# Performance work log

Hardware: AMD Instinct MI355X
Metric: run time of the kernel (lower is better)

The kernel has to match this reference:

```python
import jax, jax.numpy as jnp
import numpy as np

D = 512          # descriptor_dim
H = 8            # num_heads
HD = D // H      # per-head dim
L = 12           # GNN layers: ['self','cross']*6
NAMES = ['self', 'cross'] * 6
SINKHORN_ITERS = 100
IN_EPS = 1e-5    # InstanceNorm1d eps


def _conv1x1(W, b, x):
    # W: [o, d], b: [o], x: [b, d, n] -> [b, o, n]  (1x1 Conv1d)
    return jnp.einsum('od,bdn->bon', W, x) + b[:, None]


def _instance_norm(x):
    # InstanceNorm1d(affine=False): normalize each (batch, channel) over n
    mean = jnp.mean(x, axis=-1, keepdims=True)
    var = jnp.mean(jnp.square(x - mean), axis=-1, keepdims=True)  # biased
    return (x - mean) * jax.lax.rsqrt(var + IN_EPS)


def _mha(x, src, Wq, bq, Wk, bk, Wv, bv, Wm, bm):
    # x, src: [b, D, n] / [b, D, m]; fused head-major QKV projections
    b, _, n = x.shape
    m = src.shape[2]
    q = _conv1x1(Wq, bq, x).reshape(b, H, HD, n)
    k = _conv1x1(Wk, bk, src).reshape(b, H, HD, m)
    v = _conv1x1(Wv, bv, src).reshape(b, H, HD, m)
    scores = jnp.einsum('bhdn,bhdm->bhnm', q, k) / np.float32(np.sqrt(HD))
    prob = jax.nn.softmax(scores, axis=-1)
    out = jnp.einsum('bhnm,bhdm->bhdn', prob, v)      # [b, h, hd, n]
    # torch stacks heads at dim=2 -> [b, hd, h, n], then views (b, hd*h, n):
    out = out.transpose(0, 2, 1, 3).reshape(b, D, n)  # dim-major merge order
    return _conv1x1(Wm, bm, out)


def _prop_layer(x, src, Wq, bq, Wk, bk, Wv, bv, Wm, bm, W1, b1, W2, b2):
    # AttentionalPropagation: attn message + MLP([2D, 2D, D]) with InstanceNorm
    msg = _mha(x, src, Wq, bq, Wk, bk, Wv, bv, Wm, bm)
    y = jnp.concatenate([x, msg], axis=1)             # [b, 2D, n]
    z = jax.nn.relu(_instance_norm(_conv1x1(W1, b1, y)))
    return _conv1x1(W2, b2, z)                        # [b, D, n]


def _log_optimal_transport(scores, alpha, iters):
    b, m, n = scores.shape
    ms = jnp.asarray(m, scores.dtype)
    ns = jnp.asarray(n, scores.dtype)
    bins0 = jnp.broadcast_to(alpha, (b, m, 1))
    bins1 = jnp.broadcast_to(alpha, (b, 1, n))
    a = jnp.broadcast_to(alpha, (b, 1, 1))
    couplings = jnp.concatenate(
        [jnp.concatenate([scores, bins0], -1),
         jnp.concatenate([bins1, a], -1)], 1)         # [b, m+1, n+1]
    norm = -jnp.log(ms + ns)
    log_mu = jnp.concatenate([jnp.full((m,), norm), (jnp.log(ns) + norm)[None]])
    log_nu = jnp.concatenate([jnp.full((n,), norm), (jnp.log(ms) + norm)[None]])
    log_mu = jnp.broadcast_to(log_mu, (b, m + 1))
    log_nu = jnp.broadcast_to(log_nu, (b, n + 1))

    def step(carry, _):
        u, v = carry
        u = log_mu - jax.scipy.special.logsumexp(couplings + v[:, None, :], axis=2)
        v = log_nu - jax.scipy.special.logsumexp(couplings + u[:, :, None], axis=1)
        return (u, v), None

    (u, v), _ = jax.lax.scan(
        step, (jnp.zeros_like(log_mu), jnp.zeros_like(log_nu)), None,
        length=iters)
    return couplings + u[:, :, None] + v[:, None, :] - norm


def setup_inputs() -> dict:
    key = jax.random.key(0)
    ks = jax.random.split(key, 12)
    B, N0, N1 = 4, 1024, 1024
    s = np.float32(0.03)  # ~1/sqrt(D) init scale for stability over 12 layers

    def p(k, shape):
        return jax.random.normal(k, shape, jnp.float32) * s

    return {
        'descs_0': jax.random.normal(ks[0], (B, N0, D), jnp.float32),
        'descs_1': jax.random.normal(ks[1], (B, N1, D), jnp.float32),
        'Wq': p(ks[2], (L, D, D)), 'bq': jnp.zeros((L, D), jnp.float32),
        'Wk': p(ks[3], (L, D, D)), 'bk': jnp.zeros((L, D), jnp.float32),
        'Wv': p(ks[4], (L, D, D)), 'bv': jnp.zeros((L, D), jnp.float32),
        'Wm': p(ks[5], (L, D, D)), 'bm': jnp.zeros((L, D), jnp.float32),
        'W1': p(ks[6], (L, 2 * D, 2 * D)), 'b1': jnp.zeros((L, 2 * D), jnp.float32),
        'W2': p(ks[7], (L, D, 2 * D)), 'b2': jnp.zeros((L, D), jnp.float32),
        'Wf': p(ks[8], (D, D)), 'bf': jnp.zeros((D,), jnp.float32),
        'bin_score': jnp.asarray(1.0, jnp.float32),
    }


def reference(descs_0, descs_1, Wq, bq, Wk, bk, Wv, bv, Wm, bm,
              W1, b1, W2, b2, Wf, bf, bin_score):
    # [B, N, D] -> channels-first [B, D, N]
    x0 = jnp.transpose(descs_0, (0, 2, 1))
    x1 = jnp.transpose(descs_1, (0, 2, 1))
    for i, name in enumerate(NAMES):
        s0, s1 = (x1, x0) if name == 'cross' else (x0, x1)
        args = (Wq[i], bq[i], Wk[i], bk[i], Wv[i], bv[i], Wm[i], bm[i],
                W1[i], b1[i], W2[i], b2[i])
        d0 = _prop_layer(x0, s0, *args)
        d1 = _prop_layer(x1, s1, *args)
        x0 = x0 + d0
        x1 = x1 + d1
    m0 = _conv1x1(Wf, bf, x0)
    m1 = _conv1x1(Wf, bf, x1)
    scores = jnp.einsum('bdn,bdm->bnm', m0, m1) / np.float32(np.sqrt(D))
    return _log_optimal_transport(scores, bin_score, SINKHORN_ITERS)
```

## Files before the change

kernel.cpp:

```cpp
#include <hip/hip_runtime.h>
#include <hip/hip_bf16.h>
#include <hip/hip_fp16.h>
#include <cmath>

using bf16 = __hip_bfloat16;
typedef __attribute__((ext_vector_type(8))) short short8;
typedef __attribute__((ext_vector_type(4))) float floatx4;
typedef unsigned long long u64t;

__device__ __forceinline__ void lds_load16(void* lds, const void* g) {
  __builtin_amdgcn_global_load_lds(
      (const __attribute__((address_space(1))) void*)g,
      (__attribute__((address_space(3))) void*)lds, 16, 0, 0);
}

struct GemmP {
  const bf16* A; const bf16* B;
  int M, N, K, lda, ldb;
  long sAimg, sAh, sBimg, sBh;
  int ZH, cross;
  float scale;
  const float* bias;
  float* Cf; int ldcf; long sCfImg, sCfH;
  bf16* Cb; int ldcb; long sCbImg, sCbH;
  __half* Ch; int ldch; long sChImg, sChH;
  const float* resid;
};

template <int NTILE>
__global__ __launch_bounds__(256, 2)
void gemm_bt(GemmP p) {
  __shared__ __align__(16) bf16 As[128 * 32];
  __shared__ __align__(16) bf16 Bs[NTILE * 32];
  constexpr int MI = (NTILE == 128) ? 4 : 2;
  const int z = blockIdx.z;
  const int imgA = z / p.ZH;
  const int h = z - imgA * p.ZH;
  const int imgB = imgA ^ p.cross;
  const bf16* Ab = p.A + (long)imgA * p.sAimg + (long)h * p.sAh;
  const bf16* Bb = p.B + (long)imgB * p.sBimg + (long)h * p.sBh;
  const int m0 = blockIdx.y * 128, n0 = blockIdx.x * NTILE;
  const int t = threadIdx.x, w = t >> 6, l = t & 63;
  const int lr = l >> 2, lk = (l & 3) * 8;
  const int fr = l & 15, fk = (l >> 4) * 8;

  const bf16* aG0 = Ab + (long)(m0 + w * 16 + lr) * p.lda + lk;
  const bf16* aG1 = aG0 + (long)64 * p.lda;
  const bf16* bG0 = Bb + (long)(n0 + w * 16 + lr) * p.ldb + lk;
  const bf16* bG1 = bG0 + (long)64 * p.ldb;
  bf16* aL0 = &As[w * 16 * 32];
  bf16* aL1 = &As[(w + 4) * 16 * 32];
  bf16* bL0 = &Bs[w * 16 * 32];
  bf16* bL1 = &Bs[(w + 4) * 16 * 32];
  const int wr = (NTILE == 128) ? (w >> 1) * 64 : w * 32;
  const int wc = (NTILE == 128) ? (w & 1) * 64 : 0;

  floatx4 zero4 = {0.f, 0.f, 0.f, 0.f};
  floatx4 acc[MI][4];
#pragma unroll
  for (int i = 0; i < MI; i++)
#pragma unroll
    for (int j = 0; j < 4; j++) acc[i][j] = zero4;

  for (int k0 = 0; k0 < p.K; k0 += 32) {
    lds_load16(aL0, aG0 + k0);
    lds_load16(aL1, aG1 + k0);
    lds_load16(bL0, bG0 + k0);
    if (NTILE == 128) lds_load16(bL1, bG1 + k0);
    __syncthreads();
    short8 af[MI], bfv[4];
#pragma unroll
    for (int i = 0; i < MI; i++)
      af[i] = *(const short8*)&As[(wr + i * 16 + fr) * 32 + fk];
#pragma unroll
    for (int j = 0; j < 4; j++)
      bfv[j] = *(const short8*)&Bs[(wc + j * 16 + fr) * 32 + fk];
#pragma unroll
    for (int i = 0; i < MI; i++)
#pragma unroll
      for (int j = 0; j < 4; j++)
        acc[i][j] = __builtin_amdgcn_mfma_f32_16x16x32_bf16(af[i], bfv[j], acc[i][j], 0, 0, 0);
    __syncthreads();
  }

  const int cl = l & 15, rq = (l >> 4) * 4;
  const long cfBase = (long)imgA * p.sCfImg + (long)h * p.sCfH;
  const long cbBase = (long)imgA * p.sCbImg + (long)h * p.sCbH;
  const long chBase = (long)imgA * p.sChImg + (long)h * p.sChH;
#pragma unroll
  for (int j = 0; j < 4; j++) {
    const int col = n0 + wc + j * 16 + cl;
    if (col >= p.N) continue;
    const float bv = p.bias ? p.bias[col] : 0.f;
#pragma unroll
    for (int i = 0; i < MI; i++) {
#pragma unroll
      for (int r = 0; r < 4; r++) {
        const int row = m0 + wr + i * 16 + rq + r;
        float val = acc[i][j][r] * p.scale + bv;
        if (p.resid) val += p.resid[cfBase + (long)row * p.ldcf + col];
        if (p.Cf) p.Cf[cfBase + (long)row * p.ldcf + col] = val;
        if (p.Cb) p.Cb[cbBase + (long)row * p.ldcb + col] = __float2bfloat16(val);
        if (p.Ch) p.Ch[chBase + (long)row * p.ldch + col] = __float2half(val);
      }
    }
  }
}

__global__ __launch_bounds__(256, 2)
void attn_fused(const bf16* __restrict__ QKV, const bf16* __restrict__ vchan,
                bf16* __restrict__ Yb, int cross) {
  __shared__ __align__(16) bf16 Qs[128 * 64];
  __shared__ __align__(16) bf16 Ks[64 * 64];
  __shared__ __align__(16) bf16 Vs[64 * 64];
  __shared__ __align__(16) bf16 Ps[128 * 64];
  const int z = blockIdx.z;
  const int img = z >> 3, h = z & 7;
  const int imgB = img ^ cross;
  const int q0 = blockIdx.x * 128;
  const int t = threadIdx.x, w = t >> 6, l = t & 63;
  const int g = l >> 4, fr = l & 15;
  const int wr = w * 32;

  {
    const bf16* src = QKV + ((long)(img * 1024 + q0)) * 1536 + h * 64;
#pragma unroll
    for (int k = 0; k < 4; k++) {
      const int chunk = t + k * 256;
      const int row = chunk >> 3, c16 = chunk & 7;
      const short8 vd = *(const short8*)(src + (long)row * 1536 + c16 * 8);
      *(short8*)((char*)Qs + row * 128 + ((c16 * 16) ^ ((row & 7) << 4))) = vd;
    }
  }
  __syncthreads();

  short8 qf[2][2];
#pragma unroll
  for (int i = 0; i < 2; i++)
#pragma unroll
    for (int ks = 0; ks < 2; ks++) {
      const int row = wr + i * 16 + fr;
      qf[i][ks] = *(const short8*)((const char*)Qs + row * 128 +
                                   ((ks * 64 + g * 16) ^ ((row & 7) << 4)));
    }

  floatx4 zero4 = {0.f, 0.f, 0.f, 0.f};
  floatx4 Oa[2][4];
  float m_run[2][4], l_run[2][4];
#pragma unroll
  for (int i = 0; i < 2; i++)
#pragma unroll
    for (int r = 0; r < 4; r++) { m_run[i][r] = -3.0e38f; l_run[i][r] = 0.f; }
#pragma unroll
  for (int i = 0; i < 2; i++)
#pragma unroll
    for (int jd = 0; jd < 4; jd++) Oa[i][jd] = zero4;

  const bf16* ksrc0 = QKV + ((long)(imgB * 1024)) * 1536 + 512 + h * 64;
  const bf16* vsrc0 = vchan + (long)imgB * 524288 + (long)(h * 64) * 1024;

  for (int kv = 0; kv < 16; kv++) {
    const int kv0 = kv * 64;
#pragma unroll
    for (int k = 0; k < 2; k++) {
      const int ch = t + k * 256;
      const int row = ch >> 3, c16 = ch & 7;
      const short8 vd = *(const short8*)(ksrc0 + (long)(kv0 + row) * 1536 + c16 * 8);
      *(short8*)((char*)Ks + row * 128 + ((c16 * 16) ^ ((row & 7) << 4))) = vd;
    }
#pragma unroll
    for (int k = 0; k < 2; k++) {
      const int ch = t + k * 256;
      const int row = ch >> 3, c16 = ch & 7;
      const short8 vd = *(const short8*)(vsrc0 + (long)row * 1024 + kv0 + c16 * 8);
      *(short8*)((char*)Vs + row * 128 + ((c16 * 16) ^ ((row & 7) << 4))) = vd;
    }
    __syncthreads();

    floatx4 sa[2][4];
#pragma unroll
    for (int i = 0; i < 2; i++)
#pragma unroll
      for (int j = 0; j < 4; j++) sa[i][j] = zero4;
    short8 bk[4][2];
#pragma unroll
    for (int j = 0; j < 4; j++)
#pragma unroll
      for (int ks = 0; ks < 2; ks++) {
        const int row = j * 16 + fr;
        bk[j][ks] = *(const short8*)((const char*)Ks + row * 128 +
                                     ((ks * 64 + g * 16) ^ ((row & 7) << 4)));
      }
#pragma unroll
    for (int i = 0; i < 2; i++)
#pragma unroll
      for (int j = 0; j < 4; j++)
#pragma unroll
        for (int ks = 0; ks < 2; ks++)
          sa[i][j] = __builtin_amdgcn_mfma_f32_16x16x32_bf16(qf[i][ks], bk[j][ks], sa[i][j], 0, 0, 0);

#pragma unroll
    for (int i = 0; i < 2; i++) {
#pragma unroll
      for (int r = 0; r < 4; r++) {
        float mx = -3.0e38f;
#pragma unroll
        for (int j = 0; j < 4; j++) {
          sa[i][j][r] *= 0.125f;
          mx = fmaxf(mx, sa[i][j][r]);
        }
#pragma unroll
        for (int o = 1; o < 16; o <<= 1) mx = fmaxf(mx, __shfl_xor(mx, o));
        const float mnew = fmaxf(m_run[i][r], mx);
        const float corr = __expf(m_run[i][r] - mnew);
        m_run[i][r] = mnew;
        float ps = 0.f;
#pragma unroll
        for (int j = 0; j < 4; j++) {
          const float pv = __expf(sa[i][j][r] - mnew);
          sa[i][j][r] = pv;
          ps += pv;
        }
#pragma unroll
        for (int o = 1; o < 16; o <<= 1) ps += __shfl_xor(ps, o);
        l_run[i][r] = l_run[i][r] * corr + ps;
#pragma unroll
        for (int jd = 0; jd < 4; jd++) Oa[i][jd][r] *= corr;
      }
    }

#pragma unroll
    for (int i = 0; i < 2; i++)
#pragma unroll
      for (int j = 0; j < 4; j++)
#pragma unroll
        for (int r = 0; r < 4; r++) {
          const int row = wr + i * 16 + g * 4 + r;
          const int colB = j * 32 + fr * 2;
          *(bf16*)((char*)Ps + row * 128 + (colB ^ ((row & 7) << 4))) =
              __float2bfloat16(sa[i][j][r]);
        }

    short8 pf[2][2], vf[4][2];
#pragma unroll
    for (int i = 0; i < 2; i++)
#pragma unroll
      for (int ks = 0; ks < 2; ks++) {
        const int row = wr + i * 16 + fr;
        pf[i][ks] = *(const short8*)((const char*)Ps + row * 128 +
                                     ((ks * 64 + g * 16) ^ ((row & 7) << 4)));
      }
#pragma unroll
    for (int jd = 0; jd < 4; jd++)
#pragma unroll
      for (int ks = 0; ks < 2; ks++) {
        const int row = jd * 16 + fr;
        vf[jd][ks] = *(const short8*)((const char*)Vs + row * 128 +
                                      ((ks * 64 + g * 16) ^ ((row & 7) << 4)));
      }
#pragma unroll
    for (int i = 0; i < 2; i++)
#pragma unroll
      for (int jd = 0; jd < 4; jd++)
#pragma unroll
        for (int ks = 0; ks < 2; ks++)
          Oa[i][jd] = __builtin_amdgcn_mfma_f32_16x16x32_bf16(pf[i][ks], vf[jd][ks], Oa[i][jd], 0, 0, 0);
    __syncthreads();
  }

#pragma unroll
  for (int i = 0; i < 2; i++) {
#pragma unroll
    for (int r = 0; r < 4; r++) {
      const float inv = 1.f / l_run[i][r];
      const int qrow = q0 + wr + i * 16 + g * 4 + r;
      bf16* dst = Yb + ((long)img * 1024 + qrow) * 1024 + 512 + h * 64;
#pragma unroll
      for (int jd = 0; jd < 4; jd++)
        dst[jd * 16 + fr] = __float2bfloat16(Oa[i][jd][r] * inv);
    }
  }
}

__global__ __launch_bounds__(256)
void cvt_f2b(const float* __restrict__ in, bf16* __restrict__ out, long n) {
  long i = (long)blockIdx.x * 256 + threadIdx.x;
  const long stride = (long)gridDim.x * 256;
  for (; i < n; i += stride) out[i] = __float2bfloat16(in[i]);
}

__global__ __launch_bounds__(256)
void cvt_prep(const float* __restrict__ W1, const float* __restrict__ Wm,
              bf16* __restrict__ w1r, bf16* __restrict__ wmT) {
  const long i = (long)blockIdx.x * 256 + threadIdx.x;
  if (i < 6291456L) {
    const int lay = (int)(i >> 19);
    const long r = i & 524287;
    const int o = (int)(r >> 9), k = (int)(r & 511);
    w1r[i] = __float2bfloat16(W1[(long)lay * 1048576 + (long)o * 1024 + 512 + k]);
  } else if (i < 9437184L) {
    const long j = i - 6291456L;
    const int lay = (int)(j >> 18);
    const long r = j & 262143;
    const int c = (int)(r >> 9), ii = (int)(r & 511);
    wmT[j] = __float2bfloat16(Wm[(long)lay * 262144 + (long)ii * 512 + (c & 63) * 8 + (c >> 6)]);
  }
}

__global__ __launch_bounds__(256)
void bc_calc(const float* __restrict__ W1, const float* __restrict__ bm,
             const float* __restrict__ b1, float* __restrict__ bc) {
  const int w = threadIdx.x >> 6, l = threadIdx.x & 63;
  const int og = blockIdx.x * 4 + w;
  const int lay = og >> 10, o = og & 1023;
  const float* wrow = W1 + (long)lay * 1048576 + (long)o * 1024 + 512;
  const float* bmr = bm + lay * 512;
  float s = 0.f;
#pragma unroll
  for (int j = 0; j < 8; j++) s += wrow[l + 64 * j] * bmr[l + 64 * j];
#pragma unroll
  for (int o2 = 32; o2 >= 1; o2 >>= 1) s += __shfl_xor(s, o2);
  if (l == 0) bc[og] = b1[og] + s;
}

__global__ __launch_bounds__(256)
void cvt_layer(const float* __restrict__ Wq, const float* __restrict__ Wk,
               const float* __restrict__ Wv, const float* __restrict__ W1,
               const float* __restrict__ W2, const bf16* __restrict__ wcAll,
               const float* __restrict__ bq, const float* __restrict__ bk,
               const float* __restrict__ bv,
               int layer, bf16* __restrict__ out, float* __restrict__ bqkv) {
  const long i = (long)blockIdx.x * 256 + threadIdx.x;
  if (i >= 2359296L + 1536) return;
  if (i >= 2359296L) {
    const int j = (int)(i - 2359296L);
    float b;
    if (j < 512) b = bq[layer * 512 + j];
    else if (j < 1024) b = bk[layer * 512 + j - 512];
    else b = bv[layer * 512 + j - 1024];
    bqkv[j] = b;
    return;
  }
  if (i < 786432) {
    float v;
    if (i < 262144) v = Wq[(long)layer * 262144 + i];
    else if (i < 524288) v = Wk[(long)layer * 262144 + i - 262144];
    else v = Wv[(long)layer * 262144 + i - 524288];
    out[i] = __float2bfloat16(v);
  } else if (i < 1835008) {
    const long j = i - 786432;
    const int o = (int)(j >> 10), k = (int)(j & 1023);
    if (k < 512)
      out[i] = __float2bfloat16(W1[(long)layer * 1048576 + (long)o * 1024 + k]);
    else
      out[i] = wcAll[(long)layer * 524288 + (long)o * 512 + (k - 512)];
  } else {
    const long j = i - 1835008;
    out[i] = __float2bfloat16(W2[(long)layer * 524288 + j]);
  }
}

__global__ __launch_bounds__(256)
void init_x(const float* __restrict__ d0, const float* __restrict__ d1,
            float* __restrict__ Xf, bf16* __restrict__ Yb) {
  long i = (long)blockIdx.x * 256 + threadIdx.x;
  const long stride = (long)gridDim.x * 256;
  const long n = 8L * 1024 * 512;
  for (; i < n; i += stride) {
    const int d = (int)(i & 511);
    const long nn = i >> 9;
    const int img = (int)(nn >> 10);
    const int row = (int)(nn & 1023);
    const int b = img >> 1, s = img & 1;
    const float v = (s ? d1 : d0)[((long)b * 1024 + row) * 512 + d];
    Xf[i] = v;
    Yb[(nn << 10) + d] = __float2bfloat16(v);
  }
}

__global__ __launch_bounds__(256)
void transpose_2b(const unsigned short* __restrict__ in, int ldi,
                  unsigned short* __restrict__ out) {
  __shared__ unsigned short tile[64][65];
  const int img = blockIdx.z;
  const int m0 = blockIdx.y * 64, c0 = blockIdx.x * 64;
  const int col = threadIdx.x & 63, r0 = threadIdx.x >> 6;
  const unsigned short* ip = in + ((long)img * 1024 + m0) * ldi + c0;
#pragma unroll
  for (int i = 0; i < 16; i++) { int r = r0 + i * 4; tile[r][col] = ip[(long)r * ldi + col]; }
  __syncthreads();
  unsigned short* op = out + ((long)img * 512 + c0) * 1024 + m0;
#pragma unroll
  for (int i = 0; i < 16; i++) { int r = r0 + i * 4; op[(long)r * 1024 + col] = tile[col][r]; }
}

__global__ __launch_bounds__(256)
void in_stats(const float* __restrict__ T1, float* __restrict__ stats) {
  const int img = blockIdx.z;
  const int c = blockIdx.x * 256 + threadIdx.x;
  const int nb = blockIdx.y;
  const float* p = T1 + ((long)img * 1024 + nb * 128) * 1024 + c;
  float s = 0.f, s2 = 0.f;
#pragma unroll 4
  for (int i = 0; i < 128; i++) { const float x = p[(long)i * 1024]; s += x; s2 += x * x; }
  atomicAdd(&stats[img * 2048 + c], s);
  atomicAdd(&stats[img * 2048 + 1024 + c], s2);
}

__global__ __launch_bounds__(256)
void in_apply(const float* __restrict__ T1, const float* __restrict__ stats,
              bf16* __restrict__ Z) {
  long i = (long)blockIdx.x * 256 + threadIdx.x;
  const long stride = (long)gridDim.x * 256;
  for (; i < 8L * 1024 * 1024; i += stride) {
    const int c = (int)(i & 1023);
    const int img = (int)(i >> 20);
    const float mean = stats[img * 2048 + c] * (1.f / 1024.f);
    const float var = fmaxf(stats[img * 2048 + 1024 + c] * (1.f / 1024.f) - mean * mean, 0.f);
    const float zz = (T1[i] - mean) * rsqrtf(var + 1e-5f);
    Z[i] = __float2bfloat16(fmaxf(zz, 0.f));
  }
}

__global__ __launch_bounds__(256)
void coup_to_fp16(float* __restrict__ io, const float* __restrict__ alpha,
                  __half* __restrict__ outN, __half* __restrict__ outT) {
  __shared__ float tile[32][33];
  const float a = *alpha;
  const int b = blockIdx.z;
  const int x0 = blockIdx.x * 32, y0 = blockIdx.y * 32;
  const int lx = threadIdx.x & 31, ly = threadIdx.x >> 5;
#pragma unroll
  for (int i = 0; i < 4; i++) {
    const int y = ly + i * 8;
    if (y0 + y < 1025 && x0 + lx < 1025) {
      const long idx = ((long)b * 1025 + y0 + y) * 1025 + x0 + lx;
      const bool edge = (y0 + y == 1024) || (x0 + lx == 1024);
      float vv;
      if (edge) { vv = a; io[idx] = a; }
      else vv = io[idx];
      tile[y][lx] = vv;
      outN[idx] = __float2half(vv);
    }
  }
  __syncthreads();
#pragma unroll
  for (int i = 0; i < 4; i++) {
    const int y = ly + i * 8;
    if (x0 + y < 1025 && y0 + lx < 1025)
      outT[((long)b * 1025 + x0 + y) * 1025 + y0 + lx] = __float2half(tile[lx][y]);
  }
}

#define SK_BLOCKS 256

#define SK_ROUND(CREG, CLAST, XREG, XLAST, SRC, DST)                            \
  {                                                                             \
    u64t pr;                                                                    \
    while ((unsigned)((pr = __hip_atomic_load(&(SRC)[t], __ATOMIC_RELAXED,      \
                                              __HIP_MEMORY_SCOPE_AGENT)) >>    \
                      32) != tag)                                               \
      __builtin_amdgcn_s_sleep(1);                                              \
    sv[t] = __uint_as_float((unsigned)pr);                                      \
    if (t == 0) {                                                               \
      u64t qr;                                                                  \
      while ((unsigned)((qr = __hip_atomic_load(&(SRC)[1024], __ATOMIC_RELAXED, \
                                                __HIP_MEMORY_SCOPE_AGENT)) >>  \
                        32) != tag)                                             \
        __builtin_amdgcn_s_sleep(1);                                            \
      sv[1024] = __uint_as_float((unsigned)qr);                                 \
    }                                                                           \
    __syncthreads();                                                            \
    float M = (l == 0) ? ((CLAST) + sv[1024]) : -3.0e38f;                       \
    const float extra = M;                                                      \
    float x[16];                                                                \
    _Pragma("unroll") for (int i = 0; i < 16; i++) {                            \
      x[i] = (CREG)[i] + sv[l + 64 * i];                                        \
      M = fmaxf(M, x[i]);                                                       \
    }                                                                           \
    _Pragma("unroll") for (int o = 32; o >= 1; o >>= 1)                         \
        M = fmaxf(M, __shfl_xor(M, o));                                         \
    float S = (l == 0) ? __expf(extra - M) : 0.f;                               \
    _Pragma("unroll") for (int i = 0; i < 16; i++) S += __expf(x[i] - M);       \
    _Pragma("unroll") for (int o = 32; o >= 1; o >>= 1) S += __shfl_xor(S, o);  \
    if (l == 0) {                                                               \
      const float val = norm - (M + __logf(S));                                 \
      const u64t pk = ((u64t)(tag + 1) << 32) | (u64t)__float_as_uint(val);     \
      __hip_atomic_store(&(DST)[lw], pk, __ATOMIC_RELAXED,                      \
                         __HIP_MEMORY_SCOPE_AGENT);                             \
    }                                                                           \
    if (xtra) {                                                                 \
      float M2 = (l == 0) ? ((XLAST) + sv[1024]) : -3.0e38f;                    \
      const float e2 = M2;                                                      \
      float y[16];                                                              \
      _Pragma("unroll") for (int i = 0; i < 16; i++) {                          \
        y[i] = (XREG)[i] + sv[l + 64 * i];                                      \
        M2 = fmaxf(M2, y[i]);                                                   \
      }                                                                         \
      _Pragma("unroll") for (int o = 32; o >= 1; o >>= 1)                       \
          M2 = fmaxf(M2, __shfl_xor(M2, o));                                    \
      float S2 = (l == 0) ? __expf(e2 - M2) : 0.f;                              \
      _Pragma("unroll") for (int i = 0; i < 16; i++) S2 += __expf(y[i] - M2);   \
      _Pragma("unroll") for (int o = 32; o >= 1; o >>= 1)                       \
          S2 += __shfl_xor(S2, o);                                              \
      if (l == 0) {                                                             \
        const float v2 = (logN + norm) - (M2 + __logf(S2));                     \
        const u64t pk2 = ((u64t)(tag + 1) << 32) | (u64t)__float_as_uint(v2);   \
        __hip_atomic_store(&(DST)[1024], pk2, __ATOMIC_RELAXED,                 \
                           __HIP_MEMORY_SCOPE_AGENT);                           \
      }                                                                         \
    }                                                                           \
    tag++;                                                                      \
    __syncthreads();                                                            \
  }

__global__ __launch_bounds__(1024)
void sinkhorn_pers(const __half* __restrict__ C, const __half* __restrict__ CT,
                   u64t* __restrict__ u, u64t* __restrict__ v,
                   float norm, float logN, int iters) {
  __shared__ float sv[1025];
  const int t = threadIdx.x;
  const int w = t >> 6, l = t & 63;
  const int b = blockIdx.x >> 6;
  const int kb = blockIdx.x & 63;
  const int lw = kb * 16 + w;
  const __half* Cb = C + (long)b * 1050625;
  const __half* CTb = CT + (long)b * 1050625;
  u64t* ub = u + b * 1025;
  u64t* vb = v + b * 1025;

  float cr[16], cc[16];
  float clC, clT;
  {
    const __half* rc = Cb + (long)lw * 1025;
    const __half* rt = CTb + (long)lw * 1025;
#pragma unroll
    for (int i = 0; i < 16; i++) {
      cr[i] = __half2float(rc[l + 64 * i]);
      cc[i] = __half2float(rt[l + 64 * i]);
    }
    clC = (l == 0) ? __half2float(rc[1024]) : 0.f;
    clT = (l == 0) ? __half2float(rt[1024]) : 0.f;
  }
  const bool xtra = (lw == 0);
  float xrC[16], xrT[16], xlC = 0.f, xlT = 0.f;
  if (xtra) {
    const __half* rc = Cb + (long)1024 * 1025;
    const __half* rt = CTb + (long)1024 * 1025;
#pragma unroll
    for (int i = 0; i < 16; i++) {
      xrC[i] = __half2float(rc[l + 64 * i]);
      xrT[i] = __half2float(rt[l + 64 * i]);
    }
    if (l == 0) {
      xlC = __half2float(rc[1024]);
      xlT = __half2float(rt[1024]);
    }
  }

  unsigned tag = 0;
  for (int it = 0; it < iters; it++) {
    SK_ROUND(cr, clC, xrC, xlC, vb, ub);
    SK_ROUND(cc, clT, xrT, xlT, ub, vb);
  }
}

__global__ __launch_bounds__(256)
void ot_final(float* __restrict__ C, const u64t* __restrict__ u,
              const u64t* __restrict__ v, float norm) {
  long i = (long)blockIdx.x * 256 + threadIdx.x;
  if (i >= 4L * 1025 * 1025) return;
  const int b = (int)(i / 1050625);
  const long r = i - (long)b * 1050625;
  const int n = (int)(r / 1025);
  const int m = (int)(r - (long)n * 1025);
  const float uu = __uint_as_float((unsigned)u[b * 1025 + n]);
  const float vv = __uint_as_float((unsigned)v[b * 1025 + m]);
  C[i] += uu + vv - norm;
}

extern "C" void kernel_launch(void* const* d_in, const int* in_sizes, int n_in,
                              void* d_out, int out_size, void* d_ws, size_t ws_size,
                              hipStream_t stream) {
  (void)in_sizes; (void)n_in; (void)out_size; (void)ws_size;
  const float* descs0 = (const float*)d_in[0];
  const float* descs1 = (const float*)d_in[1];
  const float* Wq = (const float*)d_in[2];
  const float* bq = (const float*)d_in[3];
  const float* Wk = (const float*)d_in[4];
  const float* bk = (const float*)d_in[5];
  const float* Wv = (const float*)d_in[6];
  const float* bvv = (const float*)d_in[7];
  const float* Wm = (const float*)d_in[8];
  const float* bm = (const float*)d_in[9];
  const float* W1 = (const float*)d_in[10];
  const float* b1 = (const float*)d_in[11];
  const float* W2 = (const float*)d_in[12];
  const float* b2 = (const float*)d_in[13];
  const float* Wf = (const float*)d_in[14];
  const float* bff = (const float*)d_in[15];
  const float* alpha = (const float*)d_in[16];

  char* ws = (char*)d_ws;
  size_t off = 0;
  auto alloc = [&](size_t bytes) -> void* {
    off = (off + 255) & ~(size_t)255;
    void* p = ws + off;
    off += bytes;
    return p;
  };

  bf16* wL = (bf16*)alloc(2359296L * 2);
  float* bqkv = (float*)alloc(1536 * 4);
  bf16* WfB = (bf16*)alloc(512L * 512 * 2);
  bf16* wcAll = (bf16*)alloc(12L * 1024 * 512 * 2);
  float* bcAll = (float*)alloc(12L * 1024 * 4);
  float* Xf = (float*)alloc(8L * 1024 * 512 * 4);
  bf16* Yb = (bf16*)alloc(8L * 1024 * 1024 * 2);
  bf16* QKVb = (bf16*)alloc(8L * 1024 * 1536 * 2);
  bf16* vchan = (bf16*)alloc(8L * 1024 * 512 * 2);
  char* SCR = (char*)alloc(50331648);
  float* stats = (float*)alloc(12L * 16384 * 4);
  u64t* u = (u64t*)alloc(4L * 1025 * 8);
  u64t* v = (u64t*)alloc(4L * 1025 * 8);

  bf16* wqkv = wL;
  bf16* w1m = wL + 786432;
  bf16* w2 = wL + 1835008;
  float* T1 = (float*)SCR;
  bf16* Zb = (bf16*)(SCR + 33554432);
  bf16* w1rTmp = (bf16*)SCR;
  bf16* wmTTmp = (bf16*)(SCR + 12582912);
  __half* Ch = (__half*)SCR;
  __half* CTh = (__half*)(SCR + 8405248);
  bf16* mproj = (bf16*)(SCR + 33554432);
  float* coup = (float*)d_out;

  cvt_f2b<<<512, 256, 0, stream>>>(Wf, WfB, 512L * 512);
  init_x<<<4096, 256, 0, stream>>>(descs0, descs1, Xf, Yb);
  hipMemsetAsync(stats, 0, 12L * 16384 * 4, stream);

  auto gemm = [&](int ntile, const bf16* A, const bf16* B, int M, int N, int K,
                  int lda, int ldb, long sAimg, long sAh, long sBimg, long sBh,
                  int Z, int ZH, int cross, float scale, const float* bias,
                  float* Cf, int ldcf, long sCfImg, long sCfH,
                  bf16* Cb, int ldcb, long sCbImg, long sCbH,
                  __half* Ch_, int ldch, long sChImg, long sChH,
                  const float* resid) {
    GemmP p;
    p.A = A; p.B = B; p.M = M; p.N = N; p.K = K; p.lda = lda; p.ldb = ldb;
    p.sAimg = sAimg; p.sAh = sAh; p.sBimg = sBimg; p.sBh = sBh;
    p.ZH = ZH; p.cross = cross; p.scale = scale; p.bias = bias;
    p.Cf = Cf; p.ldcf = ldcf; p.sCfImg = sCfImg; p.sCfH = sCfH;
    p.Cb = Cb; p.ldcb = ldcb; p.sCbImg = sCbImg; p.sCbH = sCbH;
    p.Ch = Ch_; p.ldch = ldch; p.sChImg = sChImg; p.sChH = sChH;
    p.resid = resid;
    dim3 g((unsigned)((N + ntile - 1) / ntile), (unsigned)((M + 127) / 128), (unsigned)Z);
    if (ntile == 128) gemm_bt<128><<<g, 256, 0, stream>>>(p);
    else gemm_bt<64><<<g, 256, 0, stream>>>(p);
  };

  cvt_prep<<<36864, 256, 0, stream>>>(W1, Wm, w1rTmp, wmTTmp);
  bc_calc<<<3072, 256, 0, stream>>>(W1, bm, b1, bcAll);
  gemm(128, w1rTmp, wmTTmp, 1024, 512, 512, 512, 512, 524288, 0, 262144, 0,
       12, 1, 0, 1.f, nullptr,
       nullptr, 0, 0, 0, wcAll, 512, 524288, 0, nullptr, 0, 0, 0, nullptr);

  for (int i = 0; i < 12; i++) {
    const int cross = i & 1;
    cvt_layer<<<9222, 256, 0, stream>>>(Wq, Wk, Wv, W1, W2, wcAll, bq, bk, bvv, i, wL, bqkv);

    gemm(128, Yb, wqkv, 8192, 1536, 512, 1024, 512, 0, 0, 0, 0, 1, 1, 0, 1.f, bqkv,
         nullptr, 0, 0, 0, QKVb, 1536, 0, 0, nullptr, 0, 0, 0, nullptr);
    transpose_2b<<<dim3(8, 16, 8), 256, 0, stream>>>((const unsigned short*)(QKVb + 1024),
                                                     1536, (unsigned short*)vchan);
    attn_fused<<<dim3(8, 1, 64), 256, 0, stream>>>(QKVb, vchan, Yb, cross);

    gemm(128, Yb, w1m, 8192, 1024, 1024, 1024, 1024, 0, 0, 0, 0, 1, 1, 0, 1.f,
         bcAll + i * 1024,
         T1, 1024, 0, 0, nullptr, 0, 0, 0, nullptr, 0, 0, 0, nullptr);
    in_stats<<<dim3(4, 8, 8), 256, 0, stream>>>(T1, stats + (long)i * 16384);
    in_apply<<<8192, 256, 0, stream>>>(T1, stats + (long)i * 16384, Zb);
    gemm(128, Zb, w2, 8192, 512, 1024, 1024, 1024, 0, 0, 0, 0, 1, 1, 0, 1.f, b2 + i * 512,
         Xf, 512, 0, 0, Yb, 1024, 0, 0, nullptr, 0, 0, 0, Xf);
  }

  gemm(128, Yb, WfB, 8192, 512, 512, 1024, 512, 0, 0, 0, 0, 1, 1, 0, 1.f, bff,
       nullptr, 0, 0, 0, mproj, 512, 0, 0, nullptr, 0, 0, 0, nullptr);
  gemm(128, mproj, mproj + 524288, 1024, 1024, 512, 512, 512,
       1048576, 0, 1048576, 0, 4, 1, 0,
       0.044194173824159216f, nullptr,
       coup, 1025, 1050625, 0, nullptr, 0, 0, 0, nullptr, 0, 0, 0, nullptr);
  coup_to_fp16<<<dim3(33, 33, 4), 256, 0, stream>>>(coup, alpha, Ch, CTh);

  hipMemsetAsync(u, 0, 4L * 1025 * 8, stream);
  hipMemsetAsync(v, 0, 4L * 1025 * 8, stream);
  const float NORM = -logf(2048.f);
  const float LOGN = logf(1024.f);
  int iters = 100;
  void* args[] = {(void*)&Ch, (void*)&CTh, (void*)&u, (void*)&v,
                  (void*)&NORM, (void*)&LOGN, (void*)&iters};
  hipLaunchCooperativeKernel((void*)sinkhorn_pers, dim3(SK_BLOCKS), dim3(1024), args, 0, stream);
  ot_final<<<16417, 256, 0, stream>>>(coup, u, v, NORM);
}
```

Baseline: 3.371 ms.

## Fuse V transpose and instance-norm stats into GEMM epilogues; shrink attention tiles

The QKV GEMM epilogue now writes the V columns directly in channel-major layout, which removes the separate transpose kernel. The W1 GEMM epilogue accumulates per-channel sum and sum-of-squares with shuffles and atomics, which removes the in_stats pass that re-read T1. The attention kernel drops to 64 query rows per block with launch bounds of 4, doubling the grid to get more occupancy. The costs are strided 8-byte V stores, extra atomics, and twice as many K/V tile loads in attention.

```diff
diff --git a/kernel.cpp b/kernel.cpp
--- a/kernel.cpp
+++ b/kernel.cpp
@@ -5,6 +5,7 @@
 
 using bf16 = __hip_bfloat16;
 typedef __attribute__((ext_vector_type(8))) short short8;
+typedef __attribute__((ext_vector_type(4))) short shortx4;
 typedef __attribute__((ext_vector_type(4))) float floatx4;
 typedef unsigned long long u64t;
 
@@ -25,6 +26,8 @@
   bf16* Cb; int ldcb; long sCbImg, sCbH;
   __half* Ch; int ldch; long sChImg, sChH;
   const float* resid;
+  bf16* Cv; int vColOfs;
+  float* statsOut;
 };
 
 template <int NTILE>
@@ -92,40 +95,66 @@
     const int col = n0 + wc + j * 16 + cl;
     if (col >= p.N) continue;
     const float bv = p.bias ? p.bias[col] : 0.f;
+    const bool vcol = p.Cv && (col >= p.vColOfs);
+    float cs = 0.f, cs2 = 0.f;
 #pragma unroll
     for (int i = 0; i < MI; i++) {
+      float vr[4];
 #pragma unroll
       for (int r = 0; r < 4; r++) {
         const int row = m0 + wr + i * 16 + rq + r;
         float val = acc[i][j][r] * p.scale + bv;
         if (p.resid) val += p.resid[cfBase + (long)row * p.ldcf + col];
         if (p.Cf) p.Cf[cfBase + (long)row * p.ldcf + col] = val;
-        if (p.Cb) p.Cb[cbBase + (long)row * p.ldcb + col] = __float2bfloat16(val);
+        if (p.Cb && !vcol) p.Cb[cbBase + (long)row * p.ldcb + col] = __float2bfloat16(val);
         if (p.Ch) p.Ch[chBase + (long)row * p.ldch + col] = __float2half(val);
+        if (p.statsOut) { cs += val; cs2 += val * val; }
+        vr[r] = val;
       }
-    }
-  }
-}
-
-__global__ __launch_bounds__(256, 2)
+      if (vcol) {
+        const int row0 = m0 + wr + i * 16 + rq;
+        const int img = row0 >> 10, tok = row0 & 1023;
+        const int ch = col - p.vColOfs;
+        shortx4 pk;
+#pragma unroll
+        for (int r = 0; r < 4; r++) {
+          bf16 bb = __float2bfloat16(vr[r]);
+          pk[r] = *reinterpret_cast<short*>(&bb);
+        }
+        *(shortx4*)(p.Cv + (long)img * 524288 + (long)ch * 1024 + tok) = pk;
+      }
+    }
+    if (p.statsOut) {
+      cs += __shfl_xor(cs, 16); cs += __shfl_xor(cs, 32);
+      cs2 += __shfl_xor(cs2, 16); cs2 += __shfl_xor(cs2, 32);
+      if (l < 16) {
+        const int img = m0 >> 10;
+        atomicAdd(&p.statsOut[img * 2048 + col], cs);
+        atomicAdd(&p.statsOut[img * 2048 + 1024 + col], cs2);
+      }
+    }
+  }
+}
+
+__global__ __launch_bounds__(256, 4)
 void attn_fused(const bf16* __restrict__ QKV, const bf16* __restrict__ vchan,
                 bf16* __restrict__ Yb, int cross) {
-  __shared__ __align__(16) bf16 Qs[128 * 64];
+  __shared__ __align__(16) bf16 Qs[64 * 64];
   __shared__ __align__(16) bf16 Ks[64 * 64];
   __shared__ __align__(16) bf16 Vs[64 * 64];
-  __shared__ __align__(16) bf16 Ps[128 * 64];
+  __shared__ __align__(16) bf16 Ps[64 * 64];
   const int z = blockIdx.z;
   const int img = z >> 3, h = z & 7;
   const int imgB = img ^ cross;
-  const int q0 = blockIdx.x * 128;
+  const int q0 = blockIdx.x * 64;
   const int t = threadIdx.x, w = t >> 6, l = t & 63;
   const int g = l >> 4, fr = l & 15;
-  const int wr = w * 32;
+  const int wr = w * 16;
 
   {
     const bf16* src = QKV + ((long)(img * 1024 + q0)) * 1536 + h * 64;
 #pragma unroll
-    for (int k = 0; k < 4; k++) {
+    for (int k = 0; k < 2; k++) {
       const int chunk = t + k * 256;
       const int row = chunk >> 3, c16 = chunk & 7;
       const short8 vd = *(const short8*)(src + (long)row * 1536 + c16 * 8);
@@ -134,27 +163,21 @@
   }
   __syncthreads();
 
-  short8 qf[2][2];
-#pragma unroll
-  for (int i = 0; i < 2; i++)
-#pragma unroll
-    for (int ks = 0; ks < 2; ks++) {
-      const int row = wr + i * 16 + fr;
-      qf[i][ks] = *(const short8*)((const char*)Qs + row * 128 +
-                                   ((ks * 64 + g * 16) ^ ((row & 7) << 4)));
-    }
+  short8 qf[2];
+#pragma unroll
+  for (int ks = 0; ks < 2; ks++) {
+    const int row = wr + fr;
+    qf[ks] = *(const short8*)((const char*)Qs + row * 128 +
+                              ((ks * 64 + g * 16) ^ ((row & 7) << 4)));
+  }
 
   floatx4 zero4 = {0.f, 0.f, 0.f, 0.f};
-  floatx4 Oa[2][4];
-  float m_run[2][4], l_run[2][4];
-#pragma unroll
-  for (int i = 0; i < 2; i++)
-#pragma unroll
-    for (int r = 0; r < 4; r++) { m_run[i][r] = -3.0e38f; l_run[i][r] = 0.f; }
-#pragma unroll
-  for (int i = 0; i < 2; i++)
-#pragma unroll
-    for (int jd = 0; jd < 4; jd++) Oa[i][jd] = zero4;
+  floatx4 Oa[4];
+  float m_run[4], l_run[4];
+#pragma unroll
+  for (int r = 0; r < 4; r++) { m_run[r] = -3.0e38f; l_run[r] = 0.f; }
+#pragma unroll
+  for (int jd = 0; jd < 4; jd++) Oa[jd] = zero4;
 
   const bf16* ksrc0 = QKV + ((long)(imgB * 1024)) * 1536 + 512 + h * 64;
   const bf16* vsrc0 = vchan + (long)imgB * 524288 + (long)(h * 64) * 1024;
@@ -177,108 +200,84 @@
     }
     __syncthreads();
 
-    floatx4 sa[2][4];
-#pragma unroll
-    for (int i = 0; i < 2; i++)
-#pragma unroll
-      for (int j = 0; j < 4; j++) sa[i][j] = zero4;
-    short8 bk[4][2];
+    floatx4 sa[4];
+#pragma unroll
+    for (int j = 0; j < 4; j++) {
+      sa[j] = zero4;
+      const int row = j * 16 + fr;
+      const short8 bk0 = *(const short8*)((const char*)Ks + row * 128 +
+                                          ((g * 16) ^ ((row & 7) << 4)));
+      const short8 bk1 = *(const short8*)((const char*)Ks + row * 128 +
+                                          ((64 + g * 16) ^ ((row & 7) << 4)));
+      sa[j] = __builtin_amdgcn_mfma_f32_16x16x32_bf16(qf[0], bk0, sa[j], 0, 0, 0);
+      sa[j] = __builtin_amdgcn_mfma_f32_16x16x32_bf16(qf[1], bk1, sa[j], 0, 0, 0);
+    }
+
+#pragma unroll
+    for (int r = 0; r < 4; r++) {
+      float mx = -3.0e38f;
+#pragma unroll
+      for (int j = 0; j < 4; j++) {
+        sa[j][r] *= 0.125f;
+        mx = fmaxf(mx, sa[j][r]);
+      }
+#pragma unroll
+      for (int o = 1; o < 16; o <<= 1) mx = fmaxf(mx, __shfl_xor(mx, o));
+      const float mnew = fmaxf(m_run[r], mx);
+      const float corr = __expf(m_run[r] - mnew);
+      m_run[r] = mnew;
+      float ps = 0.f;
+#pragma unroll
+      for (int j = 0; j < 4; j++) {
+        const float pv = __expf(sa[j][r] - mnew);
+        sa[j][r] = pv;
+        ps += pv;
+      }
+#pragma unroll
+      for (int o = 1; o < 16; o <<= 1) ps += __shfl_xor(ps, o);
+      l_run[r] = l_run[r] * corr + ps;
+#pragma unroll
+      for (int jd = 0; jd < 4; jd++) Oa[jd][r] *= corr;
+    }
+
 #pragma unroll
     for (int j = 0; j < 4; j++)
 #pragma unroll
-      for (int ks = 0; ks < 2; ks++) {
-        const int row = j * 16 + fr;
-        bk[j][ks] = *(const short8*)((const char*)Ks + row * 128 +
-                                     ((ks * 64 + g * 16) ^ ((row & 7) << 4)));
+      for (int r = 0; r < 4; r++) {
+        const int row = wr + g * 4 + r;
+        const int colB = j * 32 + fr * 2;
+        *(bf16*)((char*)Ps + row * 128 + (colB ^ ((row & 7) << 4))) =
+            __float2bfloat16(sa[j][r]);
       }
-#pragma unroll
-    for (int i = 0; i < 2; i++)
-#pragma unroll
-      for (int j = 0; j < 4; j++)
-#pragma unroll
-        for (int ks = 0; ks < 2; ks++)
-          sa[i][j] = __builtin_amdgcn_mfma_f32_16x16x32_bf16(qf[i][ks], bk[j][ks], sa[i][j], 0, 0, 0);
-
-#pragma unroll
-    for (int i = 0; i < 2; i++) {
-#pragma unroll
-      for (int r = 0; r < 4; r++) {
-        float mx = -3.0e38f;
-#pragma unroll
-        for (int j = 0; j < 4; j++) {
-          sa[i][j][r] *= 0.125f;
-          mx = fmaxf(mx, sa[i][j][r]);
-        }
-#pragma unroll
-        for (int o = 1; o < 16; o <<= 1) mx = fmaxf(mx, __shfl_xor(mx, o));
-        const float mnew = fmaxf(m_run[i][r], mx);
-        const float corr = __expf(m_run[i][r] - mnew);
-        m_run[i][r] = mnew;
-        float ps = 0.f;
-#pragma unroll
-        for (int j = 0; j < 4; j++) {
-          const float pv = __expf(sa[i][j][r] - mnew);
-          sa[i][j][r] = pv;
-          ps += pv;
-        }
-#pragma unroll
-        for (int o = 1; o < 16; o <<= 1) ps += __shfl_xor(ps, o);
-        l_run[i][r] = l_run[i][r] * corr + ps;
-#pragma unroll
-        for (int jd = 0; jd < 4; jd++) Oa[i][jd][r] *= corr;
-      }
-    }
-
-#pragma unroll
-    for (int i = 0; i < 2; i++)
-#pragma unroll
-      for (int j = 0; j < 4; j++)
-#pragma unroll
-        for (int r = 0; r < 4; r++) {
-          const int row = wr + i * 16 + g * 4 + r;
-          const int colB = j * 32 + fr * 2;
-          *(bf16*)((char*)Ps + row * 128 + (colB ^ ((row & 7) << 4))) =
-              __float2bfloat16(sa[i][j][r]);
-        }
-
-    short8 pf[2][2], vf[4][2];
-#pragma unroll
-    for (int i = 0; i < 2; i++)
-#pragma unroll
-      for (int ks = 0; ks < 2; ks++) {
-        const int row = wr + i * 16 + fr;
-        pf[i][ks] = *(const short8*)((const char*)Ps + row * 128 +
-                                     ((ks * 64 + g * 16) ^ ((row & 7) << 4)));
-      }
+
+    short8 pf[2];
+#pragma unroll
+    for (int ks = 0; ks < 2; ks++) {
+      const int row = wr + fr;
+      pf[ks] = *(const short8*)((const char*)Ps + row * 128 +
+                                ((ks * 64 + g * 16) ^ ((row & 7) << 4)));
+    }
+#pragma unroll
+    for (int jd = 0; jd < 4; jd++) {
+      const int row = jd * 16 + fr;
+      const short8 vf0 = *(const short8*)((const char*)Vs + row * 128 +
+                                          ((g * 16) ^ ((row & 7) << 4)));
+      const short8 vf1 = *(const short8*)((const char*)Vs + row * 128 +
+                                          ((64 + g * 16) ^ ((row & 7) << 4)));
+      Oa[jd] = __builtin_amdgcn_mfma_f32_16x16x32_bf16(pf[0], vf0, Oa[jd], 0, 0, 0);
+      Oa[jd] = __builtin_amdgcn_mfma_f32_16x16x32_bf16(pf[1], vf1, Oa[jd], 0, 0, 0);
+    }
+    __syncthreads();
+  }
+
+#pragma unroll
+  for (int r = 0; r < 4; r++) {
+    const float inv = 1.f / l_run[r];
+    const int qrow = q0 + wr + g * 4 + r;
+    bf16* dst = Yb + ((long)img * 1024 + qrow) * 1024 + 512 + h * 64;
 #pragma unroll
     for (int jd = 0; jd < 4; jd++)
-#pragma unroll
-      for (int ks = 0; ks < 2; ks++) {
-        const int row = jd * 16 + fr;
-        vf[jd][ks] = *(const short8*)((const char*)Vs + row * 128 +
-                                      ((ks * 64 + g * 16) ^ ((row & 7) << 4)));
-      }
-#pragma unroll
-    for (int i = 0; i < 2; i++)
-#pragma unroll
-      for (int jd = 0; jd < 4; jd++)
-#pragma unroll
-        for (int ks = 0; ks < 2; ks++)
-          Oa[i][jd] = __builtin_amdgcn_mfma_f32_16x16x32_bf16(pf[i][ks], vf[jd][ks], Oa[i][jd], 0, 0, 0);
-    __syncthreads();
-  }
-
-#pragma unroll
-  for (int i = 0; i < 2; i++) {
-#pragma unroll
-    for (int r = 0; r < 4; r++) {
-      const float inv = 1.f / l_run[i][r];
-      const int qrow = q0 + wr + i * 16 + g * 4 + r;
-      bf16* dst = Yb + ((long)img * 1024 + qrow) * 1024 + 512 + h * 64;
-#pragma unroll
-      for (int jd = 0; jd < 4; jd++)
-        dst[jd * 16 + fr] = __float2bfloat16(Oa[i][jd][r] * inv);
-    }
+      dst[jd * 16 + fr] = __float2bfloat16(Oa[jd][r] * inv);
   }
 }
 
@@ -376,35 +375,6 @@
     Xf[i] = v;
     Yb[(nn << 10) + d] = __float2bfloat16(v);
   }
-}
-
-__global__ __launch_bounds__(256)
-void transpose_2b(const unsigned short* __restrict__ in, int ldi,
-                  unsigned short* __restrict__ out) {
-  __shared__ unsigned short tile[64][65];
-  const int img = blockIdx.z;
-  const int m0 = blockIdx.y * 64, c0 = blockIdx.x * 64;
-  const int col = threadIdx.x & 63, r0 = threadIdx.x >> 6;
-  const unsigned short* ip = in + ((long)img * 1024 + m0) * ldi + c0;
-#pragma unroll
-  for (int i = 0; i < 16; i++) { int r = r0 + i * 4; tile[r][col] = ip[(long)r * ldi + col]; }
-  __syncthreads();
-  unsigned short* op = out + ((long)img * 512 + c0) * 1024 + m0;
-#pragma unroll
-  for (int i = 0; i < 16; i++) { int r = r0 + i * 4; op[(long)r * 1024 + col] = tile[col][r]; }
-}
-
-__global__ __launch_bounds__(256)
-void in_stats(const float* __restrict__ T1, float* __restrict__ stats) {
-  const int img = blockIdx.z;
-  const int c = blockIdx.x * 256 + threadIdx.x;
-  const int nb = blockIdx.y;
-  const float* p = T1 + ((long)img * 1024 + nb * 128) * 1024 + c;
-  float s = 0.f, s2 = 0.f;
-#pragma unroll 4
-  for (int i = 0; i < 128; i++) { const float x = p[(long)i * 1024]; s += x; s2 += x * x; }
-  atomicAdd(&stats[img * 2048 + c], s);
-  atomicAdd(&stats[img * 2048 + 1024 + c], s2);
 }
 
 __global__ __launch_bounds__(256)
@@ -646,7 +616,7 @@
                   float* Cf, int ldcf, long sCfImg, long sCfH,
                   bf16* Cb, int ldcb, long sCbImg, long sCbH,
                   __half* Ch_, int ldch, long sChImg, long sChH,
-                  const float* resid) {
+                  const float* resid, bf16* Cv, int vColOfs, float* statsOut) {
     GemmP p;
     p.A = A; p.B = B; p.M = M; p.N = N; p.K = K; p.lda = lda; p.ldb = ldb;
     p.sAimg = sAimg; p.sAh = sAh; p.sBimg = sBimg; p.sBh = sBh;
@@ -654,7 +624,7 @@
     p.Cf = Cf; p.ldcf = ldcf; p.sCfImg = sCfImg; p.sCfH = sCfH;
     p.Cb = Cb; p.ldcb = ldcb; p.sCbImg = sCbImg; p.sCbH = sCbH;
     p.Ch = Ch_; p.ldch = ldch; p.sChImg = sChImg; p.sChH = sChH;
-    p.resid = resid;
+    p.resid = resid; p.Cv = Cv; p.vColOfs = vColOfs; p.statsOut = statsOut;
     dim3 g((unsigned)((N + ntile - 1) / ntile), (unsigned)((M + 127) / 128), (unsigned)Z);
     if (ntile == 128) gemm_bt<128><<<g, 256, 0, stream>>>(p);
     else gemm_bt<64><<<g, 256, 0, stream>>>(p);
@@ -664,33 +634,36 @@
   bc_calc<<<3072, 256, 0, stream>>>(W1, bm, b1, bcAll);
   gemm(128, w1rTmp, wmTTmp, 1024, 512, 512, 512, 512, 524288, 0, 262144, 0,
        12, 1, 0, 1.f, nullptr,
-       nullptr, 0, 0, 0, wcAll, 512, 524288, 0, nullptr, 0, 0, 0, nullptr);
+       nullptr, 0, 0, 0, wcAll, 512, 524288, 0, nullptr, 0, 0, 0,
+       nullptr, nullptr, 0, nullptr);
 
   for (int i = 0; i < 12; i++) {
     const int cross = i & 1;
     cvt_layer<<<9222, 256, 0, stream>>>(Wq, Wk, Wv, W1, W2, wcAll, bq, bk, bvv, i, wL, bqkv);
 
     gemm(128, Yb, wqkv, 8192, 1536, 512, 1024, 512, 0, 0, 0, 0, 1, 1, 0, 1.f, bqkv,
-         nullptr, 0, 0, 0, QKVb, 1536, 0, 0, nullptr, 0, 0, 0, nullptr);
-    transpose_2b<<<dim3(8, 16, 8), 256, 0, stream>>>((const unsigned short*)(QKVb + 1024),
-                                                     1536, (unsigned short*)vchan);
-    attn_fused<<<dim3(8, 1, 64), 256, 0, stream>>>(QKVb, vchan, Yb, cross);
+         nullptr, 0, 0, 0, QKVb, 1536, 0, 0, nullptr, 0, 0, 0,
+         nullptr, vchan, 1024, nullptr);
+    attn_fused<<<dim3(16, 1, 64), 256, 0, stream>>>(QKVb, vchan, Yb, cross);
 
     gemm(128, Yb, w1m, 8192, 1024, 1024, 1024, 1024, 0, 0, 0, 0, 1, 1, 0, 1.f,
          bcAll + i * 1024,
-         T1, 1024, 0, 0, nullptr, 0, 0, 0, nullptr, 0, 0, 0, nullptr);
-    in_stats<<<dim3(4, 8, 8), 256, 0, stream>>>(T1, stats + (long)i * 16384);
+         T1, 1024, 0, 0, nullptr, 0, 0, 0, nullptr, 0, 0, 0,
+         nullptr, nullptr, 0, stats + (long)i * 16384);
     in_apply<<<8192, 256, 0, stream>>>(T1, stats + (long)i * 16384, Zb);
     gemm(128, Zb, w2, 8192, 512, 1024, 1024, 1024, 0, 0, 0, 0, 1, 1, 0, 1.f, b2 + i * 512,
-         Xf, 512, 0, 0, Yb, 1024, 0, 0, nullptr, 0, 0, 0, Xf);
+         Xf, 512, 0, 0, Yb, 1024, 0, 0, nullptr, 0, 0, 0,
+         Xf, nullptr, 0, nullptr);
   }
 
   gemm(128, Yb, WfB, 8192, 512, 512, 1024, 512, 0, 0, 0, 0, 1, 1, 0, 1.f, bff,
-       nullptr, 0, 0, 0, mproj, 512, 0, 0, nullptr, 0, 0, 0, nullptr);
+       nullptr, 0, 0, 0, mproj, 512, 0, 0, nullptr, 0, 0, 0,
+       nullptr, nullptr, 0, nullptr);
   gemm(128, mproj, mproj + 524288, 1024, 1024, 512, 512, 512,
        1048576, 0, 1048576, 0, 4, 1, 0,
        0.044194173824159216f, nullptr,
-       coup, 1025, 1050625, 0, nullptr, 0, 0, 0, nullptr, 0, 0, 0, nullptr);
+       coup, 1025, 1050625, 0, nullptr, 0, 0, 0, nullptr, 0, 0, 0,
+       nullptr, nullptr, 0, nullptr);
   coup_to_fp16<<<dim3(33, 33, 4), 256, 0, stream>>>(coup, alpha, Ch, CTh);
 
   hipMemsetAsync(u, 0, 4L * 1025 * 8, stream);
```

New measurement: 3.182 ms. 1.06x faster.
